# Kernel tuning notes

Measured on AMD Instinct MI355X. Metric: run time of the kernel, lower is better.

Reference implementation:

```python
import jax, jax.numpy as jnp
import numpy as np

B, H, W, C = 32, 64, 64, 256
NH, WS, SS = 8, 8, 4
N = WS * WS
HD = C // NH
MLP_HID = 4 * C


def _rel_pos_index(ws):
    coords = np.stack(np.meshgrid(np.arange(ws), np.arange(ws), indexing='ij'))  # [2,ws,ws]
    cf = coords.reshape(2, -1)                      # [2,N]
    rc = (cf[:, :, None] - cf[:, None, :]).transpose(1, 2, 0)  # [N,N,2]
    rc[..., 0] += ws - 1
    rc[..., 1] += ws - 1
    rc[..., 0] *= 2 * ws - 1
    return rc.sum(-1)                               # [N,N] int


def _attn_mask(h, w, ws, ss):
    # Swin shifted-window mask: -100 where tokens come from different regions
    img = np.zeros((h, w))
    cnt = 0
    for hs in (slice(0, -ws), slice(-ws, -ss), slice(-ss, None)):
        for wsl in (slice(0, -ws), slice(-ws, -ss), slice(-ss, None)):
            img[hs, wsl] = cnt
            cnt += 1
    mw = img.reshape(h // ws, ws, w // ws, ws).transpose(0, 2, 1, 3).reshape(-1, ws * ws)  # [nW,N]
    diff = mw[:, None, :] - mw[:, :, None]
    return np.where(diff != 0, -100.0, 0.0).astype(np.float32)  # [nW,N,N]


_RPI = jnp.asarray(_rel_pos_index(WS))          # [N,N]
_MASK = jnp.asarray(_attn_mask(H, W, WS, SS))   # [nW,N,N]


def _ln(x, w, b, eps=1e-5):
    mu = x.mean(-1, keepdims=True)
    var = ((x - mu) ** 2).mean(-1, keepdims=True)
    return (x - mu) * jax.lax.rsqrt(var + eps) * w + b


def setup_inputs() -> dict:
    key = jax.random.key(0)
    ks = jax.random.split(key, 6)
    s = 0.02
    return {
        'x': jax.random.normal(ks[0], (B, H * W, C), jnp.float32),
        'norm1_w': jnp.ones((C,), jnp.float32),
        'norm1_b': jnp.zeros((C,), jnp.float32),
        'qkv_w': jax.random.normal(ks[1], (3 * C, C), jnp.float32) * s,
        'qkv_b': jnp.zeros((3 * C,), jnp.float32),
        'rpb_table': jax.random.normal(ks[2], ((2 * WS - 1) ** 2, NH), jnp.float32) * s,
        'proj_w': jax.random.normal(ks[3], (C, C), jnp.float32) * s,
        'proj_b': jnp.zeros((C,), jnp.float32),
        'norm2_w': jnp.ones((C,), jnp.float32),
        'norm2_b': jnp.zeros((C,), jnp.float32),
        'fc1_w': jax.random.normal(ks[4], (MLP_HID, C), jnp.float32) * s,
        'fc1_b': jnp.zeros((MLP_HID,), jnp.float32),
        'fc2_w': jax.random.normal(ks[5], (C, MLP_HID), jnp.float32) * s,
        'fc2_b': jnp.zeros((C,), jnp.float32),
    }


def reference(x, norm1_w, norm1_b, qkv_w, qkv_b, rpb_table, proj_w, proj_b,
              norm2_w, norm2_b, fc1_w, fc1_b, fc2_w, fc2_b):
    scale = HD ** -0.5
    nW = (H // WS) * (W // WS)

    shortcut = x
    h = _ln(x, norm1_w, norm1_b).reshape(B, H, W, C)
    # cyclic shift
    h = jnp.roll(h, shift=(-SS, -SS), axis=(1, 2))
    # window partition -> [B*nW, N, C]
    xw = h.reshape(B, H // WS, WS, W // WS, WS, C).transpose(0, 1, 3, 2, 4, 5).reshape(-1, N, C)

    qkv = xw @ qkv_w.T + qkv_b                      # [B*nW, N, 3C]
    qkv = qkv.reshape(-1, N, 3, NH, HD).transpose(2, 0, 3, 1, 4)  # [3, B*nW, NH, N, HD]
    q, k, v = qkv[0] * scale, qkv[1], qkv[2]

    attn = jnp.einsum('bhnd,bhmd->bhnm', q, k)      # [B*nW, NH, N, N]
    bias = rpb_table[_RPI.reshape(-1)].reshape(N, N, NH).transpose(2, 0, 1)  # [NH,N,N]
    attn = attn + bias[None]
    attn = (attn.reshape(B, nW, NH, N, N) + _MASK[None, :, None]).reshape(-1, NH, N, N)
    attn = jax.nn.softmax(attn, axis=-1)

    out = jnp.einsum('bhnm,bhmd->bhnd', attn, v)    # [B*nW, NH, N, HD]
    out = out.transpose(0, 2, 1, 3).reshape(-1, N, C)
    out = out @ proj_w.T + proj_b

    # window reverse + reverse shift
    out = out.reshape(B, H // WS, W // WS, WS, WS, C).transpose(0, 1, 3, 2, 4, 5).reshape(B, H, W, C)
    out = jnp.roll(out, shift=(SS, SS), axis=(1, 2)).reshape(B, H * W, C)

    x1 = shortcut + out
    h2 = _ln(x1, norm2_w, norm2_b)
    h2 = jax.nn.gelu(h2 @ fc1_w.T + fc1_b, approximate=False)
    h2 = h2 @ fc2_w.T + fc2_b
    return x1 + h2
```

## Files before the change

### kernel.cpp

```cpp
#include <hip/hip_runtime.h>
#include <hip/hip_bf16.h>

#define DEVI __device__ __forceinline__

using f32x4  = __attribute__((ext_vector_type(4))) float;
using bf16x8 = __attribute__((ext_vector_type(8))) short;
using s16x4  = __attribute__((ext_vector_type(4))) short;

DEVI float b2f(unsigned short u) {
  unsigned int x = ((unsigned int)u) << 16;
  return __uint_as_float(x);
}
DEVI unsigned short f2b(float f) {
  unsigned int x = __float_as_uint(f);
  unsigned int r = x + 0x7fffu + ((x >> 16) & 1u);
  return (unsigned short)(r >> 16);
}

DEVI void gload_lds16(const void* g, void* l) {
  __builtin_amdgcn_global_load_lds(
      (const __attribute__((address_space(1))) void*)g,
      (__attribute__((address_space(3))) void*)l, 16, 0, 0);
}

constexpr int kB = 32, kH = 64, kW = 64, kC = 256;
constexpr int kNH = 8, kWS = 8, kSS = 4, kN = 64, kHD = 32;
constexpr int kTOK = kB * kH * kW;
constexpr int kMLP = 4 * kC;

__global__ void conv_bf16(const float* __restrict__ src,
                          unsigned short* __restrict__ dst, int n4) {
  int i = blockIdx.x * blockDim.x + threadIdx.x;
  if (i < n4) {
    float4 v = *reinterpret_cast<const float4*>(src + (size_t)i * 4);
    s16x4 o;
    o[0] = (short)f2b(v.x); o[1] = (short)f2b(v.y);
    o[2] = (short)f2b(v.z); o[3] = (short)f2b(v.w);
    *reinterpret_cast<s16x4*>(dst + (size_t)i * 4) = o;
  }
}

__global__ __launch_bounds__(256) void ln1_shift_win(
    const float* __restrict__ x, const float* __restrict__ w,
    const float* __restrict__ bb, unsigned short* __restrict__ xw) {
  int wave = threadIdx.x >> 6, lane = threadIdx.x & 63;
  int t_dst = blockIdx.x * 4 + wave;
  int widx = t_dst >> 6, tok = t_dst & 63;
  int b = widx >> 6, win = widx & 63;
  int wh = win >> 3, ww = win & 7;
  int y = tok >> 3, xx = tok & 7;
  int r = (wh * 8 + y + kSS) & 63;
  int c = (ww * 8 + xx + kSS) & 63;
  const float* src = x + ((size_t)b * 4096 + r * 64 + c) * kC;

  float4 v = *reinterpret_cast<const float4*>(src + lane * 4);
  float s  = v.x + v.y + v.z + v.w;
  float s2 = v.x * v.x + v.y * v.y + v.z * v.z + v.w * v.w;
#pragma unroll
  for (int o = 32; o > 0; o >>= 1) {
    s  += __shfl_xor(s, o);
    s2 += __shfl_xor(s2, o);
  }
  float mu = s * (1.f / kC);
  float var = s2 * (1.f / kC) - mu * mu;
  float rstd = rsqrtf(var + 1e-5f);
  float4 wv = *reinterpret_cast<const float4*>(w + lane * 4);
  float4 bv = *reinterpret_cast<const float4*>(bb + lane * 4);
  s16x4 o;
  o[0] = (short)f2b((v.x - mu) * rstd * wv.x + bv.x);
  o[1] = (short)f2b((v.y - mu) * rstd * wv.y + bv.y);
  o[2] = (short)f2b((v.z - mu) * rstd * wv.z + bv.z);
  o[3] = (short)f2b((v.w - mu) * rstd * wv.w + bv.w);
  *reinterpret_cast<s16x4*>(xw + (size_t)t_dst * kC + lane * 4) = o;
}

template <int EPI, typename OUT_T>
__global__ __launch_bounds__(256) void gemm_bt(
    const unsigned short* __restrict__ A, const unsigned short* __restrict__ Bw,
    const float* __restrict__ bias, OUT_T* __restrict__ Co,
    const float* __restrict__ res, int M, int Nc, int K) {
  constexpr int BM = 128, BN = 128, BK = 64;
  __shared__ unsigned short sA[BM * BK];
  __shared__ unsigned short sB[BN * BK];
  int tid = threadIdx.x;
  int lane = tid & 63, wave = tid >> 6;
  int nbn = Nc / BN;
  int bm = (blockIdx.x / nbn) * BM;
  int bn = (blockIdx.x % nbn) * BN;
  int wr = wave >> 1, wc = wave & 1;

  f32x4 acc[4][4];
#pragma unroll
  for (int m = 0; m < 4; ++m)
#pragma unroll
    for (int n = 0; n < 4; ++n) acc[m][n] = (f32x4){0.f, 0.f, 0.f, 0.f};

  for (int k0 = 0; k0 < K; k0 += BK) {
#pragma unroll
    for (int it = 0; it < 4; ++it) {
      int c = it * 256 + tid;
      int row = c >> 3;
      int kc = (c & 7) * 8;
      const unsigned short* gA = A + (size_t)(bm + row) * K + k0 + kc;
      const unsigned short* gB = Bw + (size_t)(bn + row) * K + k0 + kc;
      char* lA = (char*)sA + (it * 256 + wave * 64) * 16;
      char* lB = (char*)sB + (it * 256 + wave * 64) * 16;
      gload_lds16(gA, lA);
      gload_lds16(gB, lB);
    }
    __syncthreads();
#pragma unroll
    for (int kk = 0; kk < 2; ++kk) {
      bf16x8 af[4], bfr[4];
#pragma unroll
      for (int m = 0; m < 4; ++m) {
        int row = wr * 64 + m * 16 + (lane & 15);
        af[m] = *reinterpret_cast<const bf16x8*>(
            &sA[row * BK + kk * 32 + (lane >> 4) * 8]);
      }
#pragma unroll
      for (int n = 0; n < 4; ++n) {
        int row = wc * 64 + n * 16 + (lane & 15);
        bfr[n] = *reinterpret_cast<const bf16x8*>(
            &sB[row * BK + kk * 32 + (lane >> 4) * 8]);
      }
#pragma unroll
      for (int m = 0; m < 4; ++m)
#pragma unroll
        for (int n = 0; n < 4; ++n)
          acc[m][n] = __builtin_amdgcn_mfma_f32_16x16x32_bf16(
              af[m], bfr[n], acc[m][n], 0, 0, 0);
    }
    __syncthreads();
  }

#pragma unroll
  for (int m = 0; m < 4; ++m) {
#pragma unroll
    for (int n = 0; n < 4; ++n) {
      int row0 = bm + wr * 64 + m * 16 + ((lane >> 4) << 2);
      int col = bn + wc * 64 + n * 16 + (lane & 15);
      float bcol = bias[col];
#pragma unroll
      for (int i = 0; i < 4; ++i) {
        float v = acc[m][n][i] + bcol;
        size_t idx = (size_t)(row0 + i) * Nc + col;
        if constexpr (EPI == 1) {
          v = 0.5f * v * (1.0f + erff(v * 0.70710678118654752f));
        }
        if constexpr (EPI == 2) {
          v += res[idx];
        }
        if constexpr (sizeof(OUT_T) == 2) {
          Co[idx] = (OUT_T)f2b(v);
        } else {
          Co[idx] = v;
        }
      }
    }
  }
}

__global__ __launch_bounds__(128) void attn_mfma(
    const unsigned short* __restrict__ qkv, const float* __restrict__ rpb,
    unsigned short* __restrict__ outb) {
  constexpr int PS = 72;
  __shared__ unsigned short lds[2][(64 + 32) * PS];
  int lane = threadIdx.x & 63, wave = threadIdx.x >> 6;
  int widx = blockIdx.x * 2 + wave;
  int win = widx & 63;
  int wh = win >> 3, ww = win & 7;
  unsigned short* P  = lds[wave];
  unsigned short* VT = lds[wave] + 64 * PS;
  int l15 = lane & 15, g = lane >> 4;
  int gh = g >> 1;
  size_t wbase = (size_t)widx * 64 * 768;
  constexpr float scale = 0.17677669529663687f;

  int xj = l15 & 7;
  int gxj = ww * 8 + xj;
  int rxj = gxj < 56 ? 0 : (gxj < 60 ? 1 : 2);
  int yj_[4], ryj_[4];
#pragma unroll
  for (int n = 0; n < 4; ++n) {
    yj_[n] = 2 * n + (l15 >> 3);
    int gyj = wh * 8 + yj_[n];
    ryj_[n] = gyj < 56 ? 0 : (gyj < 60 ? 1 : 2);
  }
  int rxok_[4], dx8_[4];
#pragma unroll
  for (int i = 0; i < 4; ++i) {
    int xi = (g & 1) * 4 + i;
    int gxi = ww * 8 + xi;
    int rxi = gxi < 56 ? 0 : (gxi < 60 ? 1 : 2);
    rxok_[i] = (rxi == rxj);
    dx8_[i] = (xi - xj + 7) * 8;
  }

  for (int h = 0; h < 8; ++h) {
    const unsigned short* qb = qkv + wbase + h * 32;
    bf16x8 qf[4], kf[4];
#pragma unroll
    for (int m = 0; m < 4; ++m)
      qf[m] = *reinterpret_cast<const bf16x8*>(qb + (size_t)(16 * m + l15) * 768 + g * 8);
#pragma unroll
    for (int n = 0; n < 4; ++n)
      kf[n] = *reinterpret_cast<const bf16x8*>(qb + 256 + (size_t)(16 * n + l15) * 768 + g * 8);

    f32x4 S[4][4];
#pragma unroll
    for (int m = 0; m < 4; ++m)
#pragma unroll
      for (int n = 0; n < 4; ++n) S[m][n] = (f32x4){0.f, 0.f, 0.f, 0.f};
#pragma unroll
    for (int m = 0; m < 4; ++m)
#pragma unroll
      for (int n = 0; n < 4; ++n)
        S[m][n] = __builtin_amdgcn_mfma_f32_16x16x32_bf16(qf[m], kf[n], S[m][n], 0, 0, 0);

    bf16x8 vrow[4];
#pragma unroll
    for (int i2 = 0; i2 < 4; ++i2)
      vrow[i2] = *reinterpret_cast<const bf16x8*>(qb + 512 + (size_t)lane * 768 + i2 * 8);
#pragma unroll
    for (int i2 = 0; i2 < 4; ++i2)
#pragma unroll
      for (int j = 0; j < 8; ++j)
        VT[(i2 * 8 + j) * PS + lane] = (unsigned short)vrow[i2][j];

#pragma unroll
    for (int m = 0; m < 4; ++m) {
      int yi = 2 * m + gh;
      int gyi = wh * 8 + yi;
      int ryi = gyi < 56 ? 0 : (gyi < 60 ? 1 : 2);
      int dy120_[4], rok_[4];
#pragma unroll
      for (int n = 0; n < 4; ++n) {
        dy120_[n] = (yi - yj_[n] + 7) * 120;
        rok_[n] = (ryi == ryj_[n]);
      }
#pragma unroll
      for (int i = 0; i < 4; ++i) {
        float t[4];
#pragma unroll
        for (int n = 0; n < 4; ++n) {
          float bias = rpb[dy120_[n] + dx8_[i] + h];
          float msk = (rok_[n] && rxok_[i]) ? 0.f : -100.f;
          t[n] = fmaf(S[m][n][i], scale, bias + msk);
        }
        float mx = fmaxf(fmaxf(t[0], t[1]), fmaxf(t[2], t[3]));
#pragma unroll
        for (int o = 1; o < 16; o <<= 1) mx = fmaxf(mx, __shfl_xor(mx, o));
        float sm = 0.f;
#pragma unroll
        for (int n = 0; n < 4; ++n) {
          t[n] = __expf(t[n] - mx);
          sm += t[n];
        }
#pragma unroll
        for (int o = 1; o < 16; o <<= 1) sm += __shfl_xor(sm, o);
        float rl = 1.f / sm;
        int rowoff = (16 * m + 4 * g + i) * PS;
#pragma unroll
        for (int n = 0; n < 4; ++n)
          P[rowoff + 16 * n + l15] = f2b(t[n] * rl);
      }
    }

    f32x4 O[4][2];
#pragma unroll
    for (int m = 0; m < 4; ++m)
#pragma unroll
      for (int n2 = 0; n2 < 2; ++n2) O[m][n2] = (f32x4){0.f, 0.f, 0.f, 0.f};
#pragma unroll
    for (int kk = 0; kk < 2; ++kk) {
      bf16x8 pa[4], vb[2];
#pragma unroll
      for (int m = 0; m < 4; ++m)
        pa[m] = *reinterpret_cast<const bf16x8*>(&P[(16 * m + l15) * PS + kk * 32 + g * 8]);
#pragma unroll
      for (int n2 = 0; n2 < 2; ++n2)
        vb[n2] = *reinterpret_cast<const bf16x8*>(&VT[(16 * n2 + l15) * PS + kk * 32 + g * 8]);
#pragma unroll
      for (int m = 0; m < 4; ++m)
#pragma unroll
        for (int n2 = 0; n2 < 2; ++n2)
          O[m][n2] = __builtin_amdgcn_mfma_f32_16x16x32_bf16(pa[m], vb[n2], O[m][n2], 0, 0, 0);
    }

    unsigned short* ob = outb + (size_t)widx * 64 * 256 + h * 32;
#pragma unroll
    for (int m = 0; m < 4; ++m)
#pragma unroll
      for (int n2 = 0; n2 < 2; ++n2)
#pragma unroll
        for (int i = 0; i < 4; ++i)
          ob[(16 * m + 4 * g + i) * 256 + 16 * n2 + l15] = f2b(O[m][n2][i]);
  }
}

__global__ __launch_bounds__(256) void resid_ln2(
    const float* __restrict__ x, const unsigned short* __restrict__ proj,
    const float* __restrict__ w2, const float* __restrict__ b2,
    float* __restrict__ x1out, unsigned short* __restrict__ ln2out) {
  int wave = threadIdx.x >> 6, lane = threadIdx.x & 63;
  int t = blockIdx.x * 4 + wave;
  int b = t >> 12, p = t & 4095;
  int r = p >> 6, c = p & 63;
  int rr = (r + 64 - kSS) & 63;
  int cc = (c + 64 - kSS) & 63;
  int widx = b * 64 + (rr >> 3) * 8 + (cc >> 3);
  int tok = (rr & 7) * 8 + (cc & 7);
  size_t srow = ((size_t)widx * 64 + tok) * 256;

  float4 xv = *reinterpret_cast<const float4*>(x + (size_t)t * kC + lane * 4);
  s16x4 pv = *reinterpret_cast<const s16x4*>(proj + srow + lane * 4);
  float v0 = xv.x + b2f((unsigned short)pv[0]);
  float v1 = xv.y + b2f((unsigned short)pv[1]);
  float v2 = xv.z + b2f((unsigned short)pv[2]);
  float v3 = xv.w + b2f((unsigned short)pv[3]);

  float4 o4; o4.x = v0; o4.y = v1; o4.z = v2; o4.w = v3;
  *reinterpret_cast<float4*>(x1out + (size_t)t * kC + lane * 4) = o4;

  float s = v0 + v1 + v2 + v3;
  float s2 = v0 * v0 + v1 * v1 + v2 * v2 + v3 * v3;
#pragma unroll
  for (int o = 32; o > 0; o >>= 1) {
    s  += __shfl_xor(s, o);
    s2 += __shfl_xor(s2, o);
  }
  float mu = s * (1.f / kC);
  float var = s2 * (1.f / kC) - mu * mu;
  float rstd = rsqrtf(var + 1e-5f);
  float4 wv = *reinterpret_cast<const float4*>(w2 + lane * 4);
  float4 bv = *reinterpret_cast<const float4*>(b2 + lane * 4);
  s16x4 o;
  o[0] = (short)f2b((v0 - mu) * rstd * wv.x + bv.x);
  o[1] = (short)f2b((v1 - mu) * rstd * wv.y + bv.y);
  o[2] = (short)f2b((v2 - mu) * rstd * wv.z + bv.z);
  o[3] = (short)f2b((v3 - mu) * rstd * wv.w + bv.w);
  *reinterpret_cast<s16x4*>(ln2out + (size_t)t * kC + lane * 4) = o;
}

extern "C" void kernel_launch(void* const* d_in, const int* in_sizes, int n_in,
                              void* d_out, int out_size, void* d_ws,
                              size_t ws_size, hipStream_t stream) {
  const float* x      = (const float*)d_in[0];
  const float* n1w    = (const float*)d_in[1];
  const float* n1b    = (const float*)d_in[2];
  const float* qkvw   = (const float*)d_in[3];
  const float* qkvb   = (const float*)d_in[4];
  const float* rpb    = (const float*)d_in[5];
  const float* projw  = (const float*)d_in[6];
  const float* projb  = (const float*)d_in[7];
  const float* n2w    = (const float*)d_in[8];
  const float* n2b    = (const float*)d_in[9];
  const float* fc1w   = (const float*)d_in[10];
  const float* fc1b   = (const float*)d_in[11];
  const float* fc2w   = (const float*)d_in[12];
  const float* fc2b   = (const float*)d_in[13];
  float* out = (float*)d_out;

  unsigned short* wq = (unsigned short*)d_ws;
  unsigned short* wp = wq + 768 * 256;
  unsigned short* w1 = wp + 256 * 256;
  unsigned short* w2 = w1 + 1024 * 256;
  unsigned short* bufA = w2 + 256 * 1024;
  unsigned short* bufB = bufA + (size_t)kTOK * kC;

  conv_bf16<<<192, 256, 0, stream>>>(qkvw, wq, 49152);
  conv_bf16<<<64, 256, 0, stream>>>(projw, wp, 16384);
  conv_bf16<<<256, 256, 0, stream>>>(fc1w, w1, 65536);
  conv_bf16<<<256, 256, 0, stream>>>(fc2w, w2, 65536);

  ln1_shift_win<<<kTOK / 4, 256, 0, stream>>>(x, n1w, n1b, bufA);

  gemm_bt<0, unsigned short><<<(kTOK / 128) * (768 / 128), 256, 0, stream>>>(
      bufA, wq, qkvb, bufB, nullptr, kTOK, 768, kC);

  attn_mfma<<<(kTOK / 64) / 2, 128, 0, stream>>>(bufB, rpb, bufA);

  gemm_bt<0, unsigned short><<<(kTOK / 128) * (kC / 128), 256, 0, stream>>>(
      bufA, wp, projb, bufB, nullptr, kTOK, kC, kC);

  resid_ln2<<<kTOK / 4, 256, 0, stream>>>(x, bufB, n2w, n2b, out, bufA);

  gemm_bt<1, unsigned short><<<(kTOK / 128) * (kMLP / 128), 256, 0, stream>>>(
      bufA, w1, fc1b, bufB, nullptr, kTOK, kMLP, kC);

  gemm_bt<2, float><<<(kTOK / 128) * (kC / 128), 256, 0, stream>>>(
      bufB, w2, fc2b, out, out, kTOK, kC, kMLP);
}
```

Measured before the change: 990.7 us.

## Fuse residual, reverse shift and LN2 into projection GEMM with 128x256 tiles

Replaces the GEMM with a 512-thread 128x256 tile variant using an XCD-aware block remap. The projection GEMM now does bias, residual add, reverse window/shift scatter and LayerNorm2 in its epilogue via an LDS row reduction, eliminating the separate resid_ln2 kernel and a bf16 round-trip. The fc2 GEMM scatters window-ordered rows back to image order with the residual. Larger tiles raise register pressure and reduce block count, and LN2 is written in place over the GEMM input buffer.

```diff
diff --git a/kernel.cpp b/kernel.cpp
--- a/kernel.cpp
+++ b/kernel.cpp
@@ -75,19 +75,25 @@
 }
 
 template <int EPI, typename OUT_T>
-__global__ __launch_bounds__(256) void gemm_bt(
-    const unsigned short* __restrict__ A, const unsigned short* __restrict__ Bw,
-    const float* __restrict__ bias, OUT_T* __restrict__ Co,
-    const float* __restrict__ res, int M, int Nc, int K) {
-  constexpr int BM = 128, BN = 128, BK = 64;
+__global__ __launch_bounds__(512, 4) void gemm_bt2(
+    const unsigned short* A, const unsigned short* __restrict__ Bw,
+    const float* __restrict__ bias, OUT_T* Co,
+    const float* xres, float* gx1,
+    const float* __restrict__ lnw, const float* __restrict__ lnb,
+    int M, int Nc, int K) {
+  constexpr int BM = 128, BN = 256, BK = 64;
   __shared__ unsigned short sA[BM * BK];
   __shared__ unsigned short sB[BN * BK];
+  __shared__ float redS[4][BM], redS2[4][BM];
   int tid = threadIdx.x;
   int lane = tid & 63, wave = tid >> 6;
+  int l15 = lane & 15, g = lane >> 4;
   int nbn = Nc / BN;
-  int bm = (blockIdx.x / nbn) * BM;
-  int bn = (blockIdx.x % nbn) * BN;
-  int wr = wave >> 1, wc = wave & 1;
+  int qch = gridDim.x >> 3;
+  int logical = (blockIdx.x & 7) * qch + (blockIdx.x >> 3);
+  int bm = (logical / nbn) * BM;
+  int bn = (logical % nbn) * BN;
+  int wr = wave >> 2, wc = wave & 3;
 
   f32x4 acc[4][4];
 #pragma unroll
@@ -97,33 +103,31 @@
 
   for (int k0 = 0; k0 < K; k0 += BK) {
 #pragma unroll
+    for (int it = 0; it < 2; ++it) {
+      int c = it * 512 + tid;
+      int row = c >> 3, kc = (c & 7) * 8;
+      gload_lds16(A + (size_t)(bm + row) * K + k0 + kc,
+                  (char*)sA + (it * 512 + wave * 64) * 16);
+    }
+#pragma unroll
     for (int it = 0; it < 4; ++it) {
-      int c = it * 256 + tid;
-      int row = c >> 3;
-      int kc = (c & 7) * 8;
-      const unsigned short* gA = A + (size_t)(bm + row) * K + k0 + kc;
-      const unsigned short* gB = Bw + (size_t)(bn + row) * K + k0 + kc;
-      char* lA = (char*)sA + (it * 256 + wave * 64) * 16;
-      char* lB = (char*)sB + (it * 256 + wave * 64) * 16;
-      gload_lds16(gA, lA);
-      gload_lds16(gB, lB);
+      int c = it * 512 + tid;
+      int row = c >> 3, kc = (c & 7) * 8;
+      gload_lds16(Bw + (size_t)(bn + row) * K + k0 + kc,
+                  (char*)sB + (it * 512 + wave * 64) * 16);
     }
     __syncthreads();
 #pragma unroll
     for (int kk = 0; kk < 2; ++kk) {
       bf16x8 af[4], bfr[4];
 #pragma unroll
-      for (int m = 0; m < 4; ++m) {
-        int row = wr * 64 + m * 16 + (lane & 15);
+      for (int m = 0; m < 4; ++m)
         af[m] = *reinterpret_cast<const bf16x8*>(
-            &sA[row * BK + kk * 32 + (lane >> 4) * 8]);
-      }
-#pragma unroll
-      for (int n = 0; n < 4; ++n) {
-        int row = wc * 64 + n * 16 + (lane & 15);
+            &sA[(wr * 64 + m * 16 + l15) * BK + kk * 32 + g * 8]);
+#pragma unroll
+      for (int n = 0; n < 4; ++n)
         bfr[n] = *reinterpret_cast<const bf16x8*>(
-            &sB[row * BK + kk * 32 + (lane >> 4) * 8]);
-      }
+            &sB[(wc * 64 + n * 16 + l15) * BK + kk * 32 + g * 8]);
 #pragma unroll
       for (int m = 0; m < 4; ++m)
 #pragma unroll
@@ -134,27 +138,95 @@
     __syncthreads();
   }
 
-#pragma unroll
-  for (int m = 0; m < 4; ++m) {
-#pragma unroll
-    for (int n = 0; n < 4; ++n) {
-      int row0 = bm + wr * 64 + m * 16 + ((lane >> 4) << 2);
-      int col = bn + wc * 64 + n * 16 + (lane & 15);
-      float bcol = bias[col];
+  if constexpr (EPI == 0 || EPI == 1) {
+#pragma unroll
+    for (int m = 0; m < 4; ++m) {
+#pragma unroll
+      for (int n = 0; n < 4; ++n) {
+        int row0 = bm + wr * 64 + m * 16 + g * 4;
+        int col = bn + wc * 64 + n * 16 + l15;
+        float bcol = bias[col];
+#pragma unroll
+        for (int i = 0; i < 4; ++i) {
+          float v = acc[m][n][i] + bcol;
+          if constexpr (EPI == 1)
+            v = 0.5f * v * (1.0f + erff(v * 0.70710678118654752f));
+          Co[(size_t)(row0 + i) * Nc + col] = (OUT_T)f2b(v);
+        }
+      }
+    }
+  }
+  if constexpr (EPI == 3) {
+#pragma unroll
+    for (int m = 0; m < 4; ++m) {
 #pragma unroll
       for (int i = 0; i < 4; ++i) {
-        float v = acc[m][n][i] + bcol;
-        size_t idx = (size_t)(row0 + i) * Nc + col;
-        if constexpr (EPI == 1) {
-          v = 0.5f * v * (1.0f + erff(v * 0.70710678118654752f));
-        }
-        if constexpr (EPI == 2) {
-          v += res[idx];
-        }
-        if constexpr (sizeof(OUT_T) == 2) {
-          Co[idx] = (OUT_T)f2b(v);
-        } else {
-          Co[idx] = v;
+        int row_local = wr * 64 + m * 16 + g * 4 + i;
+        int trow = bm + row_local;
+        int widx = trow >> 6, tok = trow & 63;
+        int b = widx >> 6, win = widx & 63;
+        int rr = ((win >> 3) << 3) | (tok >> 3);
+        int cc = ((win & 7) << 3) | (tok & 7);
+        int r = (rr + kSS) & 63, c2 = (cc + kSS) & 63;
+        size_t orow = ((size_t)(b << 12) + (r << 6) + c2) * 256;
+        float rs = 0.f, rs2 = 0.f;
+#pragma unroll
+        for (int n = 0; n < 4; ++n) {
+          int col = wc * 64 + n * 16 + l15;
+          float v = acc[m][n][i] + bias[col] + xres[orow + col];
+          acc[m][n][i] = v;
+          gx1[orow + col] = v;
+          rs += v; rs2 += v * v;
+        }
+#pragma unroll
+        for (int o = 1; o < 16; o <<= 1) {
+          rs  += __shfl_xor(rs, o);
+          rs2 += __shfl_xor(rs2, o);
+        }
+        if (l15 == 0) { redS[wc][row_local] = rs; redS2[wc][row_local] = rs2; }
+      }
+    }
+    __syncthreads();
+#pragma unroll
+    for (int m = 0; m < 4; ++m) {
+#pragma unroll
+      for (int i = 0; i < 4; ++i) {
+        int row_local = wr * 64 + m * 16 + g * 4 + i;
+        int trow = bm + row_local;
+        float s  = redS[0][row_local] + redS[1][row_local] +
+                   redS[2][row_local] + redS[3][row_local];
+        float s2 = redS2[0][row_local] + redS2[1][row_local] +
+                   redS2[2][row_local] + redS2[3][row_local];
+        float mu = s * (1.f / 256.f);
+        float var = s2 * (1.f / 256.f) - mu * mu;
+        float rstd = rsqrtf(var + 1e-5f);
+#pragma unroll
+        for (int n = 0; n < 4; ++n) {
+          int col = wc * 64 + n * 16 + l15;
+          Co[(size_t)trow * 256 + col] =
+              (OUT_T)f2b((acc[m][n][i] - mu) * rstd * lnw[col] + lnb[col]);
+        }
+      }
+    }
+  }
+  if constexpr (EPI == 4) {
+#pragma unroll
+    for (int m = 0; m < 4; ++m) {
+#pragma unroll
+      for (int i = 0; i < 4; ++i) {
+        int row_local = wr * 64 + m * 16 + g * 4 + i;
+        int trow = bm + row_local;
+        int widx = trow >> 6, tok = trow & 63;
+        int b = widx >> 6, win = widx & 63;
+        int rr = ((win >> 3) << 3) | (tok >> 3);
+        int cc = ((win & 7) << 3) | (tok & 7);
+        int r = (rr + kSS) & 63, c2 = (cc + kSS) & 63;
+        size_t orow = ((size_t)(b << 12) + (r << 6) + c2) * 256;
+#pragma unroll
+        for (int n = 0; n < 4; ++n) {
+          int col = wc * 64 + n * 16 + l15;
+          float v = acc[m][n][i] + bias[col] + xres[orow + col];
+          Co[orow + col] = v;
         }
       }
     }
@@ -297,50 +369,6 @@
         for (int i = 0; i < 4; ++i)
           ob[(16 * m + 4 * g + i) * 256 + 16 * n2 + l15] = f2b(O[m][n2][i]);
   }
-}
-
-__global__ __launch_bounds__(256) void resid_ln2(
-    const float* __restrict__ x, const unsigned short* __restrict__ proj,
-    const float* __restrict__ w2, const float* __restrict__ b2,
-    float* __restrict__ x1out, unsigned short* __restrict__ ln2out) {
-  int wave = threadIdx.x >> 6, lane = threadIdx.x & 63;
-  int t = blockIdx.x * 4 + wave;
-  int b = t >> 12, p = t & 4095;
-  int r = p >> 6, c = p & 63;
-  int rr = (r + 64 - kSS) & 63;
-  int cc = (c + 64 - kSS) & 63;
-  int widx = b * 64 + (rr >> 3) * 8 + (cc >> 3);
-  int tok = (rr & 7) * 8 + (cc & 7);
-  size_t srow = ((size_t)widx * 64 + tok) * 256;
-
-  float4 xv = *reinterpret_cast<const float4*>(x + (size_t)t * kC + lane * 4);
-  s16x4 pv = *reinterpret_cast<const s16x4*>(proj + srow + lane * 4);
-  float v0 = xv.x + b2f((unsigned short)pv[0]);
-  float v1 = xv.y + b2f((unsigned short)pv[1]);
-  float v2 = xv.z + b2f((unsigned short)pv[2]);
-  float v3 = xv.w + b2f((unsigned short)pv[3]);
-
-  float4 o4; o4.x = v0; o4.y = v1; o4.z = v2; o4.w = v3;
-  *reinterpret_cast<float4*>(x1out + (size_t)t * kC + lane * 4) = o4;
-
-  float s = v0 + v1 + v2 + v3;
-  float s2 = v0 * v0 + v1 * v1 + v2 * v2 + v3 * v3;
-#pragma unroll
-  for (int o = 32; o > 0; o >>= 1) {
-    s  += __shfl_xor(s, o);
-    s2 += __shfl_xor(s2, o);
-  }
-  float mu = s * (1.f / kC);
-  float var = s2 * (1.f / kC) - mu * mu;
-  float rstd = rsqrtf(var + 1e-5f);
-  float4 wv = *reinterpret_cast<const float4*>(w2 + lane * 4);
-  float4 bv = *reinterpret_cast<const float4*>(b2 + lane * 4);
-  s16x4 o;
-  o[0] = (short)f2b((v0 - mu) * rstd * wv.x + bv.x);
-  o[1] = (short)f2b((v1 - mu) * rstd * wv.y + bv.y);
-  o[2] = (short)f2b((v2 - mu) * rstd * wv.z + bv.z);
-  o[3] = (short)f2b((v3 - mu) * rstd * wv.w + bv.w);
-  *reinterpret_cast<s16x4*>(ln2out + (size_t)t * kC + lane * 4) = o;
 }
 
 extern "C" void kernel_launch(void* const* d_in, const int* in_sizes, int n_in,
@@ -376,19 +404,17 @@
 
   ln1_shift_win<<<kTOK / 4, 256, 0, stream>>>(x, n1w, n1b, bufA);
 
-  gemm_bt<0, unsigned short><<<(kTOK / 128) * (768 / 128), 256, 0, stream>>>(
-      bufA, wq, qkvb, bufB, nullptr, kTOK, 768, kC);
+  gemm_bt2<0, unsigned short><<<(kTOK / 128) * (768 / 256), 512, 0, stream>>>(
+      bufA, wq, qkvb, bufB, nullptr, nullptr, nullptr, nullptr, kTOK, 768, kC);
 
   attn_mfma<<<(kTOK / 64) / 2, 128, 0, stream>>>(bufB, rpb, bufA);
 
-  gemm_bt<0, unsigned short><<<(kTOK / 128) * (kC / 128), 256, 0, stream>>>(
-      bufA, wp, projb, bufB, nullptr, kTOK, kC, kC);
-
-  resid_ln2<<<kTOK / 4, 256, 0, stream>>>(x, bufB, n2w, n2b, out, bufA);
-
-  gemm_bt<1, unsigned short><<<(kTOK / 128) * (kMLP / 128), 256, 0, stream>>>(
-      bufA, w1, fc1b, bufB, nullptr, kTOK, kMLP, kC);
-
-  gemm_bt<2, float><<<(kTOK / 128) * (kC / 128), 256, 0, stream>>>(
-      bufB, w2, fc2b, out, out, kTOK, kC, kMLP);
-}
+  gemm_bt2<3, unsigned short><<<(kTOK / 128), 512, 0, stream>>>(
+      bufA, wp, projb, bufA, x, out, n2w, n2b, kTOK, kC, kC);
+
+  gemm_bt2<1, unsigned short><<<(kTOK / 128) * (kMLP / 256), 512, 0, stream>>>(
+      bufA, w1, fc1b, bufB, nullptr, nullptr, nullptr, nullptr, kTOK, kMLP, kC);
+
+  gemm_bt2<4, float><<<(kTOK / 128), 512, 0, stream>>>(
+      bufB, w2, fc2b, out, out, nullptr, nullptr, nullptr, kTOK, kC, kMLP);
+}
```

Result: faster. 935.6 us (-5.6%).
